# Performance work log

Hardware: AMD Instinct MI355X
Metric: run time of the kernel (lower is better)

Reference implementation:

```python
import jax, jax.numpy as jnp
import numpy as np

H = 1024      # hidden_size
NH = 16       # num_attention_heads
HD = H // NH  # attention_head_size = 64
B, S = 2, 2048


def setup_inputs() -> dict:
    key = jax.random.key(0)
    ks = jax.random.split(key, 8)
    scale = 1.0 / np.sqrt(H)
    return {
        "hidden_states": jax.random.normal(ks[0], (B, S, H), dtype=jnp.float32),
        "attention_mask": jnp.zeros((B, 1, 1, S), dtype=jnp.float32),
        "Wq": jax.random.normal(ks[1], (H, H), dtype=jnp.float32) * scale,
        "bq": jax.random.normal(ks[2], (H,), dtype=jnp.float32) * 0.02,
        "Wk": jax.random.normal(ks[3], (H, H), dtype=jnp.float32) * scale,
        "bk": jax.random.normal(ks[4], (H,), dtype=jnp.float32) * 0.02,
        "Wv": jax.random.normal(ks[5], (H, H), dtype=jnp.float32) * scale,
        "bv": jax.random.normal(ks[6], (H,), dtype=jnp.float32) * 0.02,
    }


def _split_heads(x):
    # [B,S,H] -> [B,NH,S,HD]
    b, s, _ = x.shape
    return x.reshape(b, s, NH, HD).transpose(0, 2, 1, 3)


def reference(hidden_states, attention_mask, Wq, bq, Wk, bk, Wv, bv):
    q = _split_heads(hidden_states @ Wq.T + bq)  # [B,NH,S,HD]
    k = _split_heads(hidden_states @ Wk.T + bk)
    v = _split_heads(hidden_states @ Wv.T + bv)
    scores = jnp.einsum("bhqd,bhkd->bhqk", q, k) / np.sqrt(HD).astype(np.float32)
    scores = scores + attention_mask  # additive mask, broadcast over heads/queries
    weights = jax.nn.softmax(scores, axis=-1)  # dropout is identity in eval mode
    ctx = jnp.einsum("bhqk,bhkd->bhqd", weights, v)  # [B,NH,S,HD]
    return ctx.transpose(0, 2, 1, 3).reshape(hidden_states.shape[0], hidden_states.shape[1], H)
```

## Files before the change

### kernel.cpp

```cpp
#include <hip/hip_runtime.h>
#include <hip/hip_bf16.h>
#include <math.h>

#define HSZ   1024
#define NHEAD 16
#define HDIM  64
#define BATCH 2
#define SEQ   2048

#define LOG2E 1.4426950408889634f

typedef __attribute__((ext_vector_type(8))) short short8;
typedef __attribute__((ext_vector_type(4))) short short4_t;
typedef __attribute__((ext_vector_type(4))) float floatx4;

typedef __attribute__((address_space(1))) const unsigned int gu32;
typedef __attribute__((address_space(3))) unsigned int lu32;

__device__ __forceinline__ void g2lds16(const void* g, void* l) {
    __builtin_amdgcn_global_load_lds((gu32*)g, (lu32*)l, 16, 0, 0);
}

__device__ __forceinline__ short f2bf(float f) {
    union { float f; unsigned u; } v; v.f = f;
    unsigned r = (v.u + 0x7FFF + ((v.u >> 16) & 1)) >> 16;
    return (short)r;
}

__device__ __forceinline__ unsigned pk2(float a, float b) {
    __hip_bfloat162 h = __float22bfloat162_rn(make_float2(a, b));
    return *(unsigned*)&h;
}

__device__ __forceinline__ float ex2(float x) {
#if __has_builtin(__builtin_amdgcn_exp2f)
    return __builtin_amdgcn_exp2f(x);
#else
    return exp2f(x);
#endif
}

__global__ __launch_bounds__(256) void convert_kernel(
    const float4* __restrict__ X, const float4* __restrict__ Wq,
    const float4* __restrict__ Wk, const float4* __restrict__ Wv,
    const float4* __restrict__ Mask,
    short4_t* __restrict__ Xb, short4_t* __restrict__ Wb,
    float4* __restrict__ Mw)
{
    int idx = blockIdx.x * 256 + threadIdx.x;
    if (idx >= 1835008) {
        int t = idx - 1835008;
        float4 f = Mask[t];
        float4 o;
        o.x = f.x * LOG2E; o.y = f.y * LOG2E;
        o.z = f.z * LOG2E; o.w = f.w * LOG2E;
        Mw[t] = o;
        return;
    }
    const float4* src; short4_t* dst;
    if (idx < 1048576) { src = X + idx; dst = Xb + idx; }
    else {
        int t = idx - 1048576;
        int sel = t >> 18;
        int wi  = t & 0x3FFFF;
        src = (sel == 0 ? Wq : sel == 1 ? Wk : Wv) + wi;
        dst = Wb + (sel << 18) + wi;
    }
    float4 f = *src;
    short4_t o;
    o.x = f2bf(f.x); o.y = f2bf(f.y); o.z = f2bf(f.z); o.w = f2bf(f.w);
    *dst = o;
}

__global__ __launch_bounds__(256, 3) void qkv_mfma_kernel(
    const short* __restrict__ Xb, const short* __restrict__ Wb,
    const float* __restrict__ bq, const float* __restrict__ bk,
    const float* __restrict__ bv,
    short* __restrict__ qo, short* __restrict__ ko, short* __restrict__ vT)
{
    __shared__ short Sm[128 * 132];
    short* As = Sm;
    short* Bs = Sm + 8192;

    const int tid  = threadIdx.x;
    const int lane = tid & 63;
    const int w    = tid >> 6;
    const int l    = lane & 15, quad = lane >> 4;
    const int gM   = blockIdx.y * 128;
    const int gN   = blockIdx.x * 128;
    const int wm   = (w >> 1) * 64, wn = (w & 1) * 64;
    const int ci   = lane >> 3, pb = lane & 7;

    floatx4 acc[4][4] = {};

    for (int kt = 0; kt < HSZ / 64; ++kt) {
        const int k0 = kt * 64;
        __syncthreads();
        #pragma unroll
        for (int u = 0; u < 4; ++u) {
            int c  = w * 4 + u;
            int r  = c * 8 + ci;
            int lb = pb ^ (r & 7);
            g2lds16(Xb + (size_t)(gM + r) * HSZ + k0 + lb * 8, &As[c * 512]);
            g2lds16(Wb + (size_t)(gN + r) * HSZ + k0 + lb * 8, &Bs[c * 512]);
        }
        __syncthreads();
        #pragma unroll
        for (int kk = 0; kk < 2; ++kk) {
            short8 a[4], b[4];
            #pragma unroll
            for (int i = 0; i < 4; ++i) {
                int m = wm + i * 16 + l;
                a[i] = *(const short8*)&As[m * 64 + (((quad + kk * 4) ^ (m & 7)) << 3)];
                int n = wn + i * 16 + l;
                b[i] = *(const short8*)&Bs[n * 64 + (((quad + kk * 4) ^ (n & 7)) << 3)];
            }
            #pragma unroll
            for (int i = 0; i < 4; ++i)
                #pragma unroll
                for (int j = 0; j < 4; ++j)
                    acc[i][j] = __builtin_amdgcn_mfma_f32_16x16x32_bf16(
                        a[i], b[j], acc[i][j], 0, 0, 0);
        }
    }

    const int mat = gN >> 10;

    if (mat == 2) {
        __syncthreads();
        #pragma unroll
        for (int j = 0; j < 4; ++j) {
            int fl = wn + j * 16 + l;
            float bv_ = bv[(gN & 1023) + fl];
            #pragma unroll
            for (int i = 0; i < 4; ++i)
                #pragma unroll
                for (int r = 0; r < 4; ++r)
                    Sm[fl * 132 + wm + i * 16 + quad * 4 + r]
                        = f2bf(acc[i][j][r] + bv_);
        }
        __syncthreads();
        const int bb = gM >> 11, ss0 = gM & (SEQ - 1);
        #pragma unroll
        for (int it = 0; it < 16; ++it) {
            int f = (tid >> 5) + it * 8;
            int c = (tid & 31) * 4;
            short4_t val = *(const short4_t*)&Sm[f * 132 + c];
            int b = (c >> 2) & 15;
            int cp = (c & ~63) | ((((b & 8) | ((b & 3) << 1) | ((b >> 2) & 1))) << 2);
            int nft = (gN & 1023) + f;
            int head = nft >> 6, d = nft & 63;
            *(short4_t*)&vT[(((size_t)(bb * NHEAD + head)) * HDIM + d) * SEQ
                            + ss0 + cp] = val;
        }
        return;
    }

    const float* bias = (mat == 0) ? bq : bk;
    short* dst        = (mat == 0) ? qo : ko;
    const float qscale = (mat == 0) ? 0.125f * LOG2E : 1.0f;

    #pragma unroll
    for (int j = 0; j < 4; ++j) {
        int nft = (gN & 1023) + wn + j * 16 + l;
        float bv_ = bias[nft];
        int head = nft >> 6, d = nft & 63;
        #pragma unroll
        for (int i = 0; i < 4; ++i) {
            #pragma unroll
            for (int r = 0; r < 4; ++r) {
                int gr = gM + wm + i * 16 + quad * 4 + r;
                int bb = gr >> 11, ss = gr & (SEQ - 1);
                float val = (acc[i][j][r] + bv_) * qscale;
                dst[((((size_t)bb * NHEAD + head) * SEQ + ss) << 6) + d] = f2bf(val);
            }
        }
    }
}

__global__ __launch_bounds__(256, 2) void attn_kernel(
    const short* __restrict__ Qg, const short* __restrict__ Kg,
    const short* __restrict__ VTg, const float* __restrict__ maskw,
    float* __restrict__ out)
{
    __shared__ short Qs[128 * 64];
    __shared__ alignas(16) short Ks[2][64 * 64];
    __shared__ alignas(16) short Vt[2][64 * 64];
    __shared__ alignas(16) float Ms[2][64];
    __shared__ alignas(16) float Lx[2][4][64];

    const int tid  = threadIdx.x;
    const int lane = tid & 63;
    const int w    = tid >> 6;
    const int l    = lane & 15, quad = lane >> 4;
    const int idx  = blockIdx.x;
    const int bh   = idx & 31;
    const int qt   = idx >> 5;
    const int batch = bh >> 4, head = bh & 15;
    const int qh = w & 1, kh = w >> 1;
    const int ci = lane >> 3, pb = lane & 7;

    const short* Qb = Qg + ((size_t)bh * SEQ + qt * 128) * HDIM;
    const short* Kb = Kg + (size_t)bh * SEQ * HDIM;
    const short* Vb = VTg + (size_t)bh * HDIM * SEQ;
    const float* mrow = maskw + (size_t)batch * SEQ;

    #pragma unroll
    for (int u = 0; u < 4; ++u) {
        int c = w * 4 + u;
        int r = c * 8 + ci;
        int lb = pb ^ (r & 7);
        g2lds16(Qb + (size_t)r * HDIM + lb * 8, &Qs[c * 512]);
    }
    #pragma unroll
    for (int u = 0; u < 2; ++u) {
        int c = w * 2 + u;
        int r = c * 8 + ci;
        int lb = pb ^ (r & 7);
        g2lds16(Kb + (size_t)r * HDIM + lb * 8, &Ks[0][c * 512]);
        g2lds16(Vb + (size_t)r * SEQ + lb * 8, &Vt[0][c * 512]);
    }
    if (tid < 16) g2lds16(mrow + tid * 4, &Ms[0][0]);
    __syncthreads();

    short8 aq[4][2];
    #pragma unroll
    for (int n = 0; n < 4; ++n)
        #pragma unroll
        for (int kk = 0; kk < 2; ++kk) {
            int m = qh * 64 + n * 16 + l;
            aq[n][kk] = *(const short8*)&Qs[m * 64 + (((quad + kk * 4) ^ (m & 7)) << 3)];
        }

    floatx4 o[4][4] = {};
    float l_i[4] = {0.f, 0.f, 0.f, 0.f};

    for (int kt = 0; kt < SEQ / 64; ++kt) {
        const int cur = kt & 1, nxt = cur ^ 1;
        if (kt + 1 < SEQ / 64) {
            const int r0 = (kt + 1) * 64;
            #pragma unroll
            for (int u = 0; u < 2; ++u) {
                int c = w * 2 + u;
                int r = c * 8 + ci;
                int lb = pb ^ (r & 7);
                g2lds16(Kb + (size_t)(r0 + r) * HDIM + lb * 8, &Ks[nxt][c * 512]);
                g2lds16(Vb + (size_t)r * SEQ + r0 + lb * 8, &Vt[nxt][c * 512]);
            }
            if (tid < 16) g2lds16(mrow + r0 + tid * 4, &Ms[nxt][0]);
        }

        float4 mq[2];
        #pragma unroll
        for (int m = 0; m < 2; ++m)
            mq[m] = *(const float4*)&Ms[cur][kh * 32 + m * 16 + quad * 4];

        floatx4 s[2][4];
        #pragma unroll
        for (int m = 0; m < 2; ++m) {
            floatx4 ini = {mq[m].x, mq[m].y, mq[m].z, mq[m].w};
            #pragma unroll
            for (int n = 0; n < 4; ++n) s[m][n] = ini;
        }
        #pragma unroll
        for (int kk = 0; kk < 2; ++kk) {
            short8 ak[2];
            #pragma unroll
            for (int m = 0; m < 2; ++m) {
                int kr = kh * 32 + m * 16 + l;
                ak[m] = *(const short8*)&Ks[cur][kr * 64 + (((quad + kk * 4) ^ (kr & 7)) << 3)];
            }
            #pragma unroll
            for (int m = 0; m < 2; ++m)
                #pragma unroll
                for (int n = 0; n < 4; ++n)
                    s[m][n] = __builtin_amdgcn_mfma_f32_16x16x32_bf16(
                        ak[m], aq[n][kk], s[m][n], 0, 0, 0);
        }

        #pragma unroll
        for (int n = 0; n < 4; ++n) {
            float rs = 0.f;
            #pragma unroll
            for (int m = 0; m < 2; ++m) {
                s[m][n][0] = ex2(s[m][n][0]);
                s[m][n][1] = ex2(s[m][n][1]);
                s[m][n][2] = ex2(s[m][n][2]);
                s[m][n][3] = ex2(s[m][n][3]);
                rs += (s[m][n][0] + s[m][n][1]) + (s[m][n][2] + s[m][n][3]);
            }
            l_i[n] += rs;
        }

        short8 ap[4];
        #pragma unroll
        for (int n = 0; n < 4; ++n) {
            union { unsigned u[4]; short8 s8; } pu;
            pu.u[0] = pk2(s[0][n][0], s[0][n][1]);
            pu.u[1] = pk2(s[0][n][2], s[0][n][3]);
            pu.u[2] = pk2(s[1][n][0], s[1][n][1]);
            pu.u[3] = pk2(s[1][n][2], s[1][n][3]);
            ap[n] = pu.s8;
        }

        short8 bvf[4];
        #pragma unroll
        for (int nd = 0; nd < 4; ++nd) {
            int d = nd * 16 + l;
            bvf[nd] = *(const short8*)&Vt[cur][d * 64 + (((kh * 4 + quad) ^ (d & 7)) << 3)];
        }
        #pragma unroll
        for (int nq = 0; nq < 4; ++nq)
            #pragma unroll
            for (int nd = 0; nd < 4; ++nd)
                o[nq][nd] = __builtin_amdgcn_mfma_f32_16x16x32_bf16(
                    ap[nq], bvf[nd], o[nq][nd], 0, 0, 0);

        __syncthreads();
    }

    float* reg = (qh == 0) ? (float*)&Ks[0][0] : (float*)&Vt[0][0];
    if (kh == 1) {
        #pragma unroll
        for (int nq = 0; nq < 4; ++nq)
            #pragma unroll
            for (int nd = 0; nd < 4; ++nd)
                *(floatx4*)&reg[((nq * 4 + nd) * 64 + lane) * 4] = o[nq][nd];
        #pragma unroll
        for (int n = 0; n < 4; ++n) Lx[qh][n][lane] = l_i[n];
    }
    __syncthreads();
    if (kh == 0) {
        #pragma unroll
        for (int nq = 0; nq < 4; ++nq)
            #pragma unroll
            for (int nd = 0; nd < 4; ++nd)
                o[nq][nd] += *(const floatx4*)&reg[((nq * 4 + nd) * 64 + lane) * 4];
        #pragma unroll
        for (int n = 0; n < 4; ++n) {
            float t = l_i[n] + Lx[qh][n][lane];
            t += __shfl_xor(t, 16);
            t += __shfl_xor(t, 32);
            l_i[n] = t;
        }
        #pragma unroll
        for (int nq = 0; nq < 4; ++nq) {
            #pragma unroll
            for (int r = 0; r < 4; ++r) {
                float inv = 1.0f / __shfl(l_i[nq], (lane & 48) + quad * 4 + r);
                int qrow = qt * 128 + qh * 64 + nq * 16 + quad * 4 + r;
                #pragma unroll
                for (int nd = 0; nd < 4; ++nd)
                    out[((size_t)batch * SEQ + qrow) * HSZ + head * HDIM + nd * 16 + l]
                        = o[nq][nd][r] * inv;
            }
        }
    }
}

extern "C" void kernel_launch(void* const* d_in, const int* in_sizes, int n_in,
                              void* d_out, int out_size, void* d_ws, size_t ws_size,
                              hipStream_t stream) {
    const float* hs   = (const float*)d_in[0];
    const float* mask = (const float*)d_in[1];
    const float* Wq   = (const float*)d_in[2];
    const float* bq   = (const float*)d_in[3];
    const float* Wk   = (const float*)d_in[4];
    const float* bk   = (const float*)d_in[5];
    const float* Wv   = (const float*)d_in[6];
    const float* bv   = (const float*)d_in[7];
    float* out = (float*)d_out;

    short* Xb = (short*)d_ws;
    short* Wb = Xb + 4194304;
    short* qb = Wb + 3145728;
    short* kb = qb + 4194304;
    short* vT = kb + 4194304;
    float* Mw = (float*)(vT + 4194304);

    convert_kernel<<<7172, 256, 0, stream>>>(
        (const float4*)hs, (const float4*)Wq, (const float4*)Wk, (const float4*)Wv,
        (const float4*)mask, (short4_t*)Xb, (short4_t*)Wb, (float4*)Mw);

    dim3 g2(3 * HSZ / 128, BATCH * SEQ / 128);
    qkv_mfma_kernel<<<g2, 256, 0, stream>>>(Xb, Wb, bq, bk, bv, qb, kb, vT);

    attn_kernel<<<512, 256, 0, stream>>>(qb, kb, vT, Mw, out);
}
```

Measured before the change: 153.6 us.

## Split attention over key halves with combine kernel; stage Q/K stores via LDS

The attention kernel now splits the key sequence into two halves, which doubles the grid to 1024 blocks. It writes unnormalized partial outputs and row sums to workspace, and a new combine kernel adds and normalizes them. The kernel takes no running max, so the partials combine by simple addition. LDS is unified to cut per-block shared memory, and launch bounds rise to allow more occupancy. The QKV GEMM epilogue for Q/K now transposes through LDS to issue 16-byte coalesced stores instead of scattered 2-byte stores. The cost is extra global traffic for the fp32 partials (about 32MB write plus read) and an added kernel launch.

```diff
diff --git a/kernel.cpp b/kernel.cpp
--- a/kernel.cpp
+++ b/kernel.cpp
@@ -78,7 +78,7 @@
     const float* __restrict__ bv,
     short* __restrict__ qo, short* __restrict__ ko, short* __restrict__ vT)
 {
-    __shared__ short Sm[128 * 132];
+    __shared__ short Sm[128 * 136];
     short* As = Sm;
     short* Bs = Sm + 8192;
 
@@ -125,6 +125,7 @@
     }
 
     const int mat = gN >> 10;
+    const int bb = gM >> 11, ss0 = gM & (SEQ - 1);
 
     if (mat == 2) {
         __syncthreads();
@@ -136,16 +137,15 @@
             for (int i = 0; i < 4; ++i)
                 #pragma unroll
                 for (int r = 0; r < 4; ++r)
-                    Sm[fl * 132 + wm + i * 16 + quad * 4 + r]
+                    Sm[fl * 136 + wm + i * 16 + quad * 4 + r]
                         = f2bf(acc[i][j][r] + bv_);
         }
         __syncthreads();
-        const int bb = gM >> 11, ss0 = gM & (SEQ - 1);
         #pragma unroll
         for (int it = 0; it < 16; ++it) {
             int f = (tid >> 5) + it * 8;
             int c = (tid & 31) * 4;
-            short4_t val = *(const short4_t*)&Sm[f * 132 + c];
+            short4_t val = *(const short4_t*)&Sm[f * 136 + c];
             int b = (c >> 2) & 15;
             int cp = (c & ~63) | ((((b & 8) | ((b & 3) << 1) | ((b >> 2) & 1))) << 2);
             int nft = (gN & 1023) + f;
@@ -160,32 +160,37 @@
     short* dst        = (mat == 0) ? qo : ko;
     const float qscale = (mat == 0) ? 0.125f * LOG2E : 1.0f;
 
+    __syncthreads();
     #pragma unroll
     for (int j = 0; j < 4; ++j) {
-        int nft = (gN & 1023) + wn + j * 16 + l;
-        float bv_ = bias[nft];
+        int fl = wn + j * 16 + l;
+        float bb_ = bias[(gN & 1023) + fl];
+        #pragma unroll
+        for (int i = 0; i < 4; ++i)
+            #pragma unroll
+            for (int r = 0; r < 4; ++r)
+                Sm[(wm + i * 16 + quad * 4 + r) * 136 + fl]
+                    = f2bf((acc[i][j][r] + bb_) * qscale);
+    }
+    __syncthreads();
+    #pragma unroll
+    for (int it = 0; it < 8; ++it) {
+        int row = (tid >> 4) + it * 16;
+        int fc  = (tid & 15) * 8;
+        short8 val = *(const short8*)&Sm[row * 136 + fc];
+        int nft = (gN & 1023) + fc;
         int head = nft >> 6, d = nft & 63;
-        #pragma unroll
-        for (int i = 0; i < 4; ++i) {
-            #pragma unroll
-            for (int r = 0; r < 4; ++r) {
-                int gr = gM + wm + i * 16 + quad * 4 + r;
-                int bb = gr >> 11, ss = gr & (SEQ - 1);
-                float val = (acc[i][j][r] + bv_) * qscale;
-                dst[((((size_t)bb * NHEAD + head) * SEQ + ss) << 6) + d] = f2bf(val);
-            }
-        }
-    }
-}
-
-__global__ __launch_bounds__(256, 2) void attn_kernel(
+        *(short8*)&dst[(((size_t)(bb * NHEAD + head)) * SEQ + ss0 + row) * HDIM + d]
+            = val;
+    }
+}
+
+__global__ __launch_bounds__(256, 4) void attn_kernel(
     const short* __restrict__ Qg, const short* __restrict__ Kg,
     const short* __restrict__ VTg, const float* __restrict__ maskw,
-    float* __restrict__ out)
+    float* __restrict__ Opart, float* __restrict__ Lpart)
 {
-    __shared__ short Qs[128 * 64];
-    __shared__ alignas(16) short Ks[2][64 * 64];
-    __shared__ alignas(16) short Vt[2][64 * 64];
+    __shared__ alignas(16) short Sh[4][4096];
     __shared__ alignas(16) float Ms[2][64];
     __shared__ alignas(16) float Lx[2][4][64];
 
@@ -195,30 +200,33 @@
     const int l    = lane & 15, quad = lane >> 4;
     const int idx  = blockIdx.x;
     const int bh   = idx & 31;
-    const int qt   = idx >> 5;
+    const int qt   = (idx >> 5) & 15;
+    const int ks   = idx >> 9;
     const int batch = bh >> 4, head = bh & 15;
     const int qh = w & 1, kh = w >> 1;
     const int ci = lane >> 3, pb = lane & 7;
 
     const short* Qb = Qg + ((size_t)bh * SEQ + qt * 128) * HDIM;
-    const short* Kb = Kg + (size_t)bh * SEQ * HDIM;
+    const short* Kb = Kg + ((size_t)bh * SEQ + ks * 1024) * HDIM;
     const short* Vb = VTg + (size_t)bh * HDIM * SEQ;
-    const float* mrow = maskw + (size_t)batch * SEQ;
+    const float* mrow = maskw + (size_t)batch * SEQ + ks * 1024;
+
+    short* Qst = (short*)&Sh[2][0];
 
     #pragma unroll
     for (int u = 0; u < 4; ++u) {
         int c = w * 4 + u;
         int r = c * 8 + ci;
         int lb = pb ^ (r & 7);
-        g2lds16(Qb + (size_t)r * HDIM + lb * 8, &Qs[c * 512]);
+        g2lds16(Qb + (size_t)r * HDIM + lb * 8, &Qst[c * 512]);
     }
     #pragma unroll
     for (int u = 0; u < 2; ++u) {
         int c = w * 2 + u;
         int r = c * 8 + ci;
         int lb = pb ^ (r & 7);
-        g2lds16(Kb + (size_t)r * HDIM + lb * 8, &Ks[0][c * 512]);
-        g2lds16(Vb + (size_t)r * SEQ + lb * 8, &Vt[0][c * 512]);
+        g2lds16(Kb + (size_t)r * HDIM + lb * 8, &Sh[0][c * 512]);
+        g2lds16(Vb + (size_t)r * SEQ + ks * 1024 + lb * 8, &Sh[1][c * 512]);
     }
     if (tid < 16) g2lds16(mrow + tid * 4, &Ms[0][0]);
     __syncthreads();
@@ -229,23 +237,26 @@
         #pragma unroll
         for (int kk = 0; kk < 2; ++kk) {
             int m = qh * 64 + n * 16 + l;
-            aq[n][kk] = *(const short8*)&Qs[m * 64 + (((quad + kk * 4) ^ (m & 7)) << 3)];
-        }
+            aq[n][kk] = *(const short8*)&Qst[m * 64
+                          + (((quad + kk * 4) ^ (m & 7)) << 3)];
+        }
+    __syncthreads();
 
     floatx4 o[4][4] = {};
     float l_i[4] = {0.f, 0.f, 0.f, 0.f};
 
-    for (int kt = 0; kt < SEQ / 64; ++kt) {
+    for (int kt = 0; kt < 16; ++kt) {
         const int cur = kt & 1, nxt = cur ^ 1;
-        if (kt + 1 < SEQ / 64) {
+        if (kt + 1 < 16) {
             const int r0 = (kt + 1) * 64;
             #pragma unroll
             for (int u = 0; u < 2; ++u) {
                 int c = w * 2 + u;
                 int r = c * 8 + ci;
                 int lb = pb ^ (r & 7);
-                g2lds16(Kb + (size_t)(r0 + r) * HDIM + lb * 8, &Ks[nxt][c * 512]);
-                g2lds16(Vb + (size_t)r * SEQ + r0 + lb * 8, &Vt[nxt][c * 512]);
+                g2lds16(Kb + (size_t)(r0 + r) * HDIM + lb * 8, &Sh[2 * nxt][c * 512]);
+                g2lds16(Vb + (size_t)r * SEQ + ks * 1024 + r0 + lb * 8,
+                        &Sh[2 * nxt + 1][c * 512]);
             }
             if (tid < 16) g2lds16(mrow + r0 + tid * 4, &Ms[nxt][0]);
         }
@@ -268,7 +279,8 @@
             #pragma unroll
             for (int m = 0; m < 2; ++m) {
                 int kr = kh * 32 + m * 16 + l;
-                ak[m] = *(const short8*)&Ks[cur][kr * 64 + (((quad + kk * 4) ^ (kr & 7)) << 3)];
+                ak[m] = *(const short8*)&Sh[2 * cur][kr * 64
+                            + (((quad + kk * 4) ^ (kr & 7)) << 3)];
             }
             #pragma unroll
             for (int m = 0; m < 2; ++m)
@@ -307,7 +319,8 @@
         #pragma unroll
         for (int nd = 0; nd < 4; ++nd) {
             int d = nd * 16 + l;
-            bvf[nd] = *(const short8*)&Vt[cur][d * 64 + (((kh * 4 + quad) ^ (d & 7)) << 3)];
+            bvf[nd] = *(const short8*)&Sh[2 * cur + 1][d * 64
+                          + (((kh * 4 + quad) ^ (d & 7)) << 3)];
         }
         #pragma unroll
         for (int nq = 0; nq < 4; ++nq)
@@ -319,7 +332,7 @@
         __syncthreads();
     }
 
-    float* reg = (qh == 0) ? (float*)&Ks[0][0] : (float*)&Vt[0][0];
+    float* reg = (qh == 0) ? (float*)&Sh[0][0] : (float*)&Sh[2][0];
     if (kh == 1) {
         #pragma unroll
         for (int nq = 0; nq < 4; ++nq)
@@ -343,19 +356,45 @@
             t += __shfl_xor(t, 32);
             l_i[n] = t;
         }
+        if (quad == 0) {
+            #pragma unroll
+            for (int n = 0; n < 4; ++n)
+                Lpart[((size_t)ks * 32 + bh) * SEQ + qt * 128 + qh * 64 + n * 16 + l]
+                    = l_i[n];
+        }
+        float* Od = Opart + (size_t)ks * (4096ull * 1024);
         #pragma unroll
         for (int nq = 0; nq < 4; ++nq) {
             #pragma unroll
             for (int r = 0; r < 4; ++r) {
-                float inv = 1.0f / __shfl(l_i[nq], (lane & 48) + quad * 4 + r);
                 int qrow = qt * 128 + qh * 64 + nq * 16 + quad * 4 + r;
                 #pragma unroll
                 for (int nd = 0; nd < 4; ++nd)
-                    out[((size_t)batch * SEQ + qrow) * HSZ + head * HDIM + nd * 16 + l]
-                        = o[nq][nd][r] * inv;
+                    Od[((size_t)batch * SEQ + qrow) * HSZ + head * HDIM + nd * 16 + l]
+                        = o[nq][nd][r];
             }
         }
     }
+}
+
+__global__ __launch_bounds__(256) void combine_kernel(
+    const float4* __restrict__ O0, const float4* __restrict__ O1,
+    const float* __restrict__ L, float4* __restrict__ out)
+{
+    int f = blockIdx.x * 256 + threadIdx.x;
+    int e = f << 2;
+    int h = (e >> 6) & 15;
+    int s = (e >> 10) & 2047;
+    int b = e >> 21;
+    int bh = b * 16 + h;
+    float l0 = L[(size_t)bh * SEQ + s];
+    float l1 = L[65536 + (size_t)bh * SEQ + s];
+    float inv = 1.0f / (l0 + l1);
+    float4 a = O0[f], c = O1[f];
+    float4 r;
+    r.x = (a.x + c.x) * inv; r.y = (a.y + c.y) * inv;
+    r.z = (a.z + c.z) * inv; r.w = (a.w + c.w) * inv;
+    out[f] = r;
 }
 
 extern "C" void kernel_launch(void* const* d_in, const int* in_sizes, int n_in,
@@ -376,7 +415,9 @@
     short* qb = Wb + 3145728;
     short* kb = qb + 4194304;
     short* vT = kb + 4194304;
-    float* Mw = (float*)(vT + 4194304);
+    float* Mw    = (float*)(vT + 4194304);
+    float* Opart = Mw + 4096;
+    float* Lpart = Opart + 2ull * 4194304;
 
     convert_kernel<<<7172, 256, 0, stream>>>(
         (const float4*)hs, (const float4*)Wq, (const float4*)Wk, (const float4*)Wv,
@@ -385,5 +426,9 @@
     dim3 g2(3 * HSZ / 128, BATCH * SEQ / 128);
     qkv_mfma_kernel<<<g2, 256, 0, stream>>>(Xb, Wb, bq, bk, bv, qb, kb, vT);
 
-    attn_kernel<<<512, 256, 0, stream>>>(qb, kb, vT, Mw, out);
-}
+    attn_kernel<<<1024, 256, 0, stream>>>(qb, kb, vT, Mw, Opart, Lpart);
+
+    combine_kernel<<<4096, 256, 0, stream>>>(
+        (const float4*)Opart, (const float4*)(Opart + 4194304ull),
+        Lpart, (float4*)out);
+}
```

Measured after the change: 289.9 us. +88.8%, slower.
